# Kernel optimization log

Hardware: AMD Instinct MI355X
Metric: run time of the kernel (lower is better)

## Reference

```python
import jax, jax.numpy as jnp
import numpy as np

N_NODES = 50000
N_EDGES = 625000
D = 128          # hidden_dim
H = 8            # num_heads
DH = D // H      # head_dim
L = 4            # num_layers
F_IN = 64        # in_channels
G = 64           # num graphs
BETA = 1.0
EPS = 1e-5       # layernorm eps


def _seg_softmax(s, idx, n):
    # softmax of s over segments defined by idx (segments present in idx are never empty)
    m = jax.ops.segment_max(s, idx, num_segments=n)
    e = jnp.exp(s - m[idx])
    d = jax.ops.segment_sum(e, idx, num_segments=n)
    return e / d[idx]


def _ln(x, s, b):
    mu = jnp.mean(x, axis=-1, keepdims=True)
    var = jnp.var(x, axis=-1, keepdims=True)
    return (x - mu) / jnp.sqrt(var + EPS) * s + b


def _forward(x, edge_index, batch, node_W, node_b, cW1, cb1, cW2, cb2,
             qW, qb, kW, kb, vW, vb, oW, ob, bW, bb,
             f1W, f1b, f2W, f2b, n1s, n1b, n2s, n2b,
             outW1, outb1, outW2, outb2):
    N = x.shape[0]
    src, tgt = edge_index[0], edge_index[1]
    h = x @ node_W + node_b                              # [N, D]
    for l in range(L):
        # ---- dynamic curvature (attention-approximated Wasserstein) ----
        h_src, h_tgt = h[src], h[tgt]                    # [E, D]
        sim = jnp.sum(h_src * h_tgt, axis=-1) * BETA     # [E]
        alpha = _seg_softmax(sim, tgt, N)                # segment softmax over tgt
        dist = jnp.linalg.norm(h_src - h_tgt, axis=-1)   # [E]
        agg = jax.ops.segment_sum(alpha * dist, tgt, num_segments=N)
        curv = 1.0 - agg[tgt] / jnp.maximum(dist, 1e-6)  # [E]
        ce = jax.nn.relu(curv[:, None] @ cW1 + cb1) @ cW2 + cb2  # [E, D]
        # ---- CurvphormerLayer ----
        xn = _ln(h, n1s[l], n1b[l])
        q = (xn @ qW[l] + qb[l]).reshape(N, H, DH)
        k = (xn @ kW[l] + kb[l]).reshape(N, H, DH)
        v = (xn @ vW[l] + vb[l]).reshape(N, H, DH)
        scores = jnp.sum(q[src] * k[tgt], axis=-1) / (DH ** 0.5)  # [E, H]
        scores = scores + ce @ bW[l] + bb[l]                       # curvature bias
        probs = _seg_softmax(scores, tgt, N)                       # [E, H]
        msgs = (probs[..., None] * v[tgt]).reshape(-1, D)          # [E, D]
        aggm = jax.ops.segment_sum(msgs, src, num_segments=N)     # scatter to src
        h = h + (aggm @ oW[l] + ob[l])
        xn2 = _ln(h, n2s[l], n2b[l])
        h = h + (jax.nn.relu(xn2 @ f1W[l] + f1b[l]) @ f2W[l] + f2b[l])
    # ---- mean pool per graph ----
    counts = jnp.maximum(jax.ops.segment_sum(jnp.ones((N,), h.dtype), batch, num_segments=G), 1.0)
    g = jax.ops.segment_sum(h, batch, num_segments=G) / counts[:, None]
    return jax.nn.relu(g @ outW1 + outb1) @ outW2 + outb2


def setup_inputs() -> dict:
    keys = iter(jax.random.split(jax.random.key(0), 32))
    p = lambda shape, s=0.02: jax.random.normal(next(keys), shape, jnp.float32) * s
    x = jax.random.normal(next(keys), (N_NODES, F_IN), jnp.float32)
    edge_index = jax.random.randint(next(keys), (2, N_EDGES), 0, N_NODES)
    batch = jnp.sort(jax.random.randint(next(keys), (N_NODES,), 0, G))
    inp = {
        "x": x, "edge_index": edge_index, "batch": batch,
        "node_W": p((F_IN, D)), "node_b": p((D,)),
        "cW1": p((1, D)), "cb1": p((D,)), "cW2": p((D, D)), "cb2": p((D,)),
        "qW": p((L, D, D)), "qb": p((L, D)),
        "kW": p((L, D, D)), "kb": p((L, D)),
        "vW": p((L, D, D)), "vb": p((L, D)),
        "oW": p((L, D, D)), "ob": p((L, D)),
        "bW": p((L, D, H)), "bb": p((L, H)),
        "f1W": p((L, D, 4 * D)), "f1b": p((L, 4 * D)),
        "f2W": p((L, 4 * D, D)), "f2b": p((L, D)),
        "n1s": jnp.ones((L, D), jnp.float32), "n1b": jnp.zeros((L, D), jnp.float32),
        "n2s": jnp.ones((L, D), jnp.float32), "n2b": jnp.zeros((L, D), jnp.float32),
        "outW1": p((D, D // 2)), "outb1": p((D // 2,)),
        "outW2": p((D // 2, 1)), "outb2": p((1,)),
    }
    return inp


def reference(x, edge_index, batch, node_W, node_b, cW1, cb1, cW2, cb2,
              qW, qb, kW, kb, vW, vb, oW, ob, bW, bb,
              f1W, f1b, f2W, f2b, n1s, n1b, n2s, n2b,
              outW1, outb1, outW2, outb2):
    return _forward(x, edge_index, batch, node_W, node_b, cW1, cb1, cW2, cb2,
                    qW, qb, kW, kb, vW, vb, oW, ob, bW, bb,
                    f1W, f1b, f2W, f2b, n1s, n1b, n2s, n2b,
                    outW1, outb1, outW2, outb2)
```

## Files before the change

### kernel.cpp

```cpp
#include <hip/hip_runtime.h>

#define NN 50000
#define NE 625000
#define DD 128
#define HH 8
#define DHH 16
#define NL 4
#define FIN 64
#define NG 64
#define LN_EPS 1e-5f
#define NSEG 129
#define NT32 1563
#define NT64 782
#define NBS 196

typedef __bf16 bf16x8_t __attribute__((ext_vector_type(8)));
typedef unsigned short ushort8_t __attribute__((ext_vector_type(8)));
typedef float f32x4_t __attribute__((ext_vector_type(4)));
union BF8 { ushort8_t u; bf16x8_t b; };

__device__ __forceinline__ void fma4(float4& a, float s, float4 w) {
  a.x = fmaf(s, w.x, a.x); a.y = fmaf(s, w.y, a.y);
  a.z = fmaf(s, w.z, a.z); a.w = fmaf(s, w.w, a.w);
}
__device__ __forceinline__ unsigned short f2bf(float f) {
  unsigned u = __float_as_uint(f);
  unsigned r = ((u >> 16) & 1u) + 0x7FFFu;
  return (unsigned short)((u + r) >> 16);
}
__device__ __forceinline__ float bf2f(unsigned short u) {
  return __uint_as_float((unsigned)u << 16);
}

__device__ __forceinline__ void ln_tile_bf32(const float* __restrict__ h, int nb,
                                             const float* __restrict__ sc,
                                             const float* __restrict__ bi,
                                             ushort* xbf) {
  int tid = threadIdx.x;
  int r = tid >> 4, l16 = tid & 15;
  int nr = nb + r; if (nr >= NN) nr = NN - 1;
  const float* hp = h + (size_t)nr * DD + l16 * 8;
  float4 a0 = *(const float4*)hp;
  float4 a1 = *(const float4*)(hp + 4);
  float sum = a0.x + a0.y + a0.z + a0.w + a1.x + a1.y + a1.z + a1.w;
  float sq  = a0.x*a0.x + a0.y*a0.y + a0.z*a0.z + a0.w*a0.w
            + a1.x*a1.x + a1.y*a1.y + a1.z*a1.z + a1.w*a1.w;
#pragma unroll
  for (int off = 8; off >= 1; off >>= 1) {
    sum += __shfl_xor(sum, off, 64);
    sq  += __shfl_xor(sq,  off, 64);
  }
  float mu   = sum * (1.0f / DD);
  float var  = sq * (1.0f / DD) - mu * mu;
  float rstd = rsqrtf(var + LN_EPS);
  int d0 = l16 * 8;
  float4 s0 = *(const float4*)(sc + d0), s1 = *(const float4*)(sc + d0 + 4);
  float4 b0 = *(const float4*)(bi + d0), b1 = *(const float4*)(bi + d0 + 4);
  ushort8_t u;
  u[0] = f2bf((a0.x - mu) * rstd * s0.x + b0.x);
  u[1] = f2bf((a0.y - mu) * rstd * s0.y + b0.y);
  u[2] = f2bf((a0.z - mu) * rstd * s0.z + b0.z);
  u[3] = f2bf((a0.w - mu) * rstd * s0.w + b0.w);
  u[4] = f2bf((a1.x - mu) * rstd * s1.x + b1.x);
  u[5] = f2bf((a1.y - mu) * rstd * s1.y + b1.y);
  u[6] = f2bf((a1.z - mu) * rstd * s1.z + b1.z);
  u[7] = f2bf((a1.w - mu) * rstd * s1.w + b1.w);
  int off = (r * 256 + l16 * 16) ^ ((r & 7) << 4);
  *(ushort8_t*)((char*)xbf + off) = u;
}

__device__ __forceinline__ void ln_tile_bf64(const float* __restrict__ h, int nb,
                                             const float* __restrict__ sc,
                                             const float* __restrict__ bi,
                                             ushort* xbf) {
  int tid = threadIdx.x;
  int l16 = tid & 15;
  int d0 = l16 * 8;
  float4 s0 = *(const float4*)(sc + d0), s1 = *(const float4*)(sc + d0 + 4);
  float4 b0 = *(const float4*)(bi + d0), b1 = *(const float4*)(bi + d0 + 4);
#pragma unroll
  for (int p = 0; p < 2; p++) {
    int r = p * 32 + (tid >> 4);
    int nr = nb + r; if (nr >= NN) nr = NN - 1;
    const float* hp = h + (size_t)nr * DD + d0;
    float4 a0 = *(const float4*)hp;
    float4 a1 = *(const float4*)(hp + 4);
    float sum = a0.x + a0.y + a0.z + a0.w + a1.x + a1.y + a1.z + a1.w;
    float sq  = a0.x*a0.x + a0.y*a0.y + a0.z*a0.z + a0.w*a0.w
              + a1.x*a1.x + a1.y*a1.y + a1.z*a1.z + a1.w*a1.w;
#pragma unroll
    for (int off = 8; off >= 1; off >>= 1) {
      sum += __shfl_xor(sum, off, 64);
      sq  += __shfl_xor(sq,  off, 64);
    }
    float mu   = sum * (1.0f / DD);
    float var  = sq * (1.0f / DD) - mu * mu;
    float rstd = rsqrtf(var + LN_EPS);
    ushort8_t u;
    u[0] = f2bf((a0.x - mu) * rstd * s0.x + b0.x);
    u[1] = f2bf((a0.y - mu) * rstd * s0.y + b0.y);
    u[2] = f2bf((a0.z - mu) * rstd * s0.z + b0.z);
    u[3] = f2bf((a0.w - mu) * rstd * s0.w + b0.w);
    u[4] = f2bf((a1.x - mu) * rstd * s1.x + b1.x);
    u[5] = f2bf((a1.y - mu) * rstd * s1.y + b1.y);
    u[6] = f2bf((a1.z - mu) * rstd * s1.z + b1.z);
    u[7] = f2bf((a1.w - mu) * rstd * s1.w + b1.w);
    int off = (r * 256 + l16 * 16) ^ ((r & 7) << 4);
    *(ushort8_t*)((char*)xbf + off) = u;
  }
}

__global__ __launch_bounds__(256) void k_node_proj(const float* __restrict__ x,
                                                   const float* __restrict__ W,
                                                   const float* __restrict__ b,
                                                   float* __restrict__ h) {
  __shared__ float Wl[FIN * DD];
  __shared__ float xt[32][FIN];
  int tid = threadIdx.x;
  int nb = blockIdx.x * 32;
  for (int i = tid * 4; i < FIN * DD; i += 1024)
    *(float4*)&Wl[i] = *(const float4*)(W + i);
  for (int i = tid * 4; i < 32 * FIN; i += 1024) {
    int row = i >> 6, cc = i & 63;
    int node = nb + row; if (node >= NN) node = NN - 1;
    *(float4*)&xt[row][cc] = *(const float4*)(x + (size_t)node * FIN + cc);
  }
  __syncthreads();
  int c4 = (tid & 31) * 4;
  int r0 = (tid >> 5) * 4;
  float4 bv = *(const float4*)(b + c4);
  float4 a0 = bv, a1 = bv, a2 = bv, a3 = bv;
  for (int k = 0; k < FIN; k++) {
    float4 wv = *(const float4*)&Wl[k * DD + c4];
    fma4(a0, xt[r0][k], wv);
    fma4(a1, xt[r0 + 1][k], wv);
    fma4(a2, xt[r0 + 2][k], wv);
    fma4(a3, xt[r0 + 3][k], wv);
  }
  int n0 = nb + r0;
  if (n0 < NN)     *(float4*)(h + (size_t)n0 * DD + c4) = a0;
  if (n0 + 1 < NN) *(float4*)(h + (size_t)(n0 + 1) * DD + c4) = a1;
  if (n0 + 2 < NN) *(float4*)(h + (size_t)(n0 + 2) * DD + c4) = a2;
  if (n0 + 3 < NN) *(float4*)(h + (size_t)(n0 + 3) * DD + c4) = a3;
}

__global__ __launch_bounds__(256) void k_edge1(const int* __restrict__ src_s, const int* __restrict__ tgt_s,
                                               const float* __restrict__ h, float* __restrict__ sim,
                                               float* __restrict__ dist) {
  int gid = blockIdx.x * 256 + threadIdx.x;
  int e = gid >> 4;
  if (e >= NE) return;
  int j = gid & 15;
  int s = src_s[e], t = tgt_s[e];
  const float4* ap = (const float4*)(h + (size_t)s * DD + j * 8);
  const float4* bp = (const float4*)(h + (size_t)t * DD + j * 8);
  float4 a0 = ap[0], a1 = ap[1];
  float4 b0 = bp[0], b1 = bp[1];
  float dot = 0.f, sq = 0.f;
  dot = fmaf(a0.x, b0.x, dot); dot = fmaf(a0.y, b0.y, dot);
  dot = fmaf(a0.z, b0.z, dot); dot = fmaf(a0.w, b0.w, dot);
  dot = fmaf(a1.x, b1.x, dot); dot = fmaf(a1.y, b1.y, dot);
  dot = fmaf(a1.z, b1.z, dot); dot = fmaf(a1.w, b1.w, dot);
  float d0 = a0.x - b0.x, d1 = a0.y - b0.y, d2 = a0.z - b0.z, d3 = a0.w - b0.w;
  float d4 = a1.x - b1.x, d5 = a1.y - b1.y, d6 = a1.z - b1.z, d7 = a1.w - b1.w;
  sq = fmaf(d0, d0, sq); sq = fmaf(d1, d1, sq); sq = fmaf(d2, d2, sq); sq = fmaf(d3, d3, sq);
  sq = fmaf(d4, d4, sq); sq = fmaf(d5, d5, sq); sq = fmaf(d6, d6, sq); sq = fmaf(d7, d7, sq);
#pragma unroll
  for (int off = 8; off >= 1; off >>= 1) {
    dot += __shfl_xor(dot, off, 64);
    sq  += __shfl_xor(sq,  off, 64);
  }
  if (j == 0) {
    sim[e]  = dot;
    dist[e] = sqrtf(sq);
  }
}

__global__ __launch_bounds__(256) void k_curva(const int* __restrict__ rowstart_t,
    const int* __restrict__ eid_t, const float* __restrict__ sim,
    const float* __restrict__ dist, float* __restrict__ aggv) {
  int node = blockIdx.x * 32 + (threadIdx.x >> 3);
  if (node >= NN) return;
  int j = threadIdx.x & 7;
  int rs = rowstart_t[node], re = rowstart_t[node + 1];
  float m = -3.4e38f;
  for (int i = rs + j; i < re; i += 8) m = fmaxf(m, sim[eid_t[i]]);
#pragma unroll
  for (int off = 1; off <= 4; off <<= 1) m = fmaxf(m, __shfl_xor(m, off, 64));
  float den = 0.f, nd = 0.f;
  for (int i = rs + j; i < re; i += 8) {
    int e = eid_t[i];
    float ev = expf(sim[e] - m);
    den += ev;
    nd = fmaf(ev, dist[e], nd);
  }
#pragma unroll
  for (int off = 1; off <= 4; off <<= 1) {
    den += __shfl_xor(den, off, 64);
    nd  += __shfl_xor(nd,  off, 64);
  }
  if (j == 0) aggv[node] = den > 0.f ? nd / den : 0.f;
}

__global__ __launch_bounds__(512) void k_ln_qkv(const float* __restrict__ h,
    const float* __restrict__ n1s_l, const float* __restrict__ n1b_l,
    const ushort* __restrict__ qkvT_l,
    const float* __restrict__ qb_l, const float* __restrict__ kb_l, const float* __restrict__ vb_l,
    ushort* __restrict__ q, ushort* __restrict__ kk, ushort* __restrict__ v) {
  __shared__ __align__(16) ushort xbf[32 * DD];
  int nb = blockIdx.x * 32;
  ln_tile_bf32(h, nb, n1s_l, n1b_l, xbf);
  __syncthreads();
  int lane = threadIdx.x & 63;
  int w = threadIdx.x >> 6;
  int g = lane >> 4, c = lane & 15;
  int xr = (c & 7) << 4;
  char* xb = (char*)xbf;
  BF8 a[2][4];
#pragma unroll
  for (int nt = 0; nt < 2; nt++)
#pragma unroll
    for (int kt = 0; kt < 4; kt++)
      a[nt][kt].u = *(ushort8_t*)(xb + (((nt * 16 + c) * 256 + kt * 64 + g * 16) ^ xr));
#pragma unroll
  for (int ti = 0; ti < 3; ti++) {
    int t = w * 3 + ti;
    int m = t >> 3;
    int colb = (t & 7) * 16;
    const float* bias = (m == 0 ? qb_l : (m == 1 ? kb_l : vb_l));
    float4 bv = *(const float4*)(bias + colb + g * 4);
    f32x4_t acc0 = {bv.x, bv.y, bv.z, bv.w};
    f32x4_t acc1 = acc0;
    const ushort* wp = qkvT_l + (size_t)(m * DD + colb + c) * DD + g * 8;
#pragma unroll
    for (int kt = 0; kt < 4; kt++) {
      BF8 b; b.u = *(const ushort8_t*)(wp + kt * 32);
      acc0 = __builtin_amdgcn_mfma_f32_16x16x32_bf16(b.b, a[0][kt].b, acc0, 0, 0, 0);
      acc1 = __builtin_amdgcn_mfma_f32_16x16x32_bf16(b.b, a[1][kt].b, acc1, 0, 0, 0);
    }
    ushort* out = (m == 0 ? q : (m == 1 ? kk : v));
    int n0 = nb + c;
    if (n0 < NN) {
      ushort4 o; o.x = f2bf(acc0[0]); o.y = f2bf(acc0[1]); o.z = f2bf(acc0[2]); o.w = f2bf(acc0[3]);
      *(ushort4*)(out + (size_t)n0 * DD + colb + g * 4) = o;
    }
    int n1 = nb + 16 + c;
    if (n1 < NN) {
      ushort4 o; o.x = f2bf(acc1[0]); o.y = f2bf(acc1[1]); o.z = f2bf(acc1[2]); o.w = f2bf(acc1[3]);
      *(ushort4*)(out + (size_t)n1 * DD + colb + g * 4) = o;
    }
  }
}

__global__ __launch_bounds__(256) void k_scores(const int* __restrict__ src_s, const int* __restrict__ tgt_s,
    const ushort* __restrict__ q, const ushort* __restrict__ k,
    const float* __restrict__ dist, const float* __restrict__ aggv,
    const float* __restrict__ bp_g,
    const float* __restrict__ slope_l, const float* __restrict__ inter_l,
    float* __restrict__ escore) {
  __shared__ float lsl[NSEG * HH], lin[NSEG * HH], bp[DD];
  __shared__ float lcurv[32];
  __shared__ int   lseg[32];
  int tid = threadIdx.x;
  for (int idx = tid; idx < NSEG * HH; idx += 256) { lsl[idx] = slope_l[idx]; lin[idx] = inter_l[idx]; }
  if (tid < DD) bp[tid] = bp_g[tid];
  __syncthreads();
  int eb = blockIdx.x * 32;
  if (tid < 32) {
    int e = eb + tid;
    if (e < NE) {
      int t = tgt_s[e];
      float curv = 1.0f - aggv[t] / fmaxf(dist[e], 1e-6f);
      int lo = 0, hi = DD;
      while (lo < hi) { int mid = (lo + hi) >> 1; if (bp[mid] < curv) lo = mid + 1; else hi = mid; }
      lcurv[tid] = curv;
      lseg[tid] = lo;
    }
  }
  __syncthreads();
  int gi = blockIdx.x * 256 + tid;
  if (gi >= NE * HH) return;
  int i = gi >> 3, hh = gi & 7;
  int s = src_s[i], t = tgt_s[i];
  int li = tid >> 3;
  float curv = lcurv[li];
  int seg = lseg[li];
  float bias = fmaf(lsl[seg * HH + hh], curv, lin[seg * HH + hh]);
  const ushort8_t* qp = (const ushort8_t*)(q + (size_t)s * DD + hh * DHH);
  const ushort8_t* kp = (const ushort8_t*)(k + (size_t)t * DD + hh * DHH);
  float dot = 0.f;
#pragma unroll
  for (int ii = 0; ii < 2; ii++) {
    ushort8_t a = qp[ii], b = kp[ii];
#pragma unroll
    for (int jj = 0; jj < 8; jj++) dot = fmaf(bf2f(a[jj]), bf2f(b[jj]), dot);
  }
  escore[gi] = dot * 0.25f + bias;
  (void)t;
}

__global__ __launch_bounds__(256) void k_softmax_t(const int* __restrict__ rowstart_t,
    const int* __restrict__ eid_t, const float* __restrict__ escore, float2* __restrict__ msd) {
  int node = blockIdx.x * 32 + (threadIdx.x >> 3);
  if (node >= NN) return;
  int hh = threadIdx.x & 7;
  int rs = rowstart_t[node], re = rowstart_t[node + 1];
  float m = -3.4e38f;
  int i = rs;
  for (; i + 4 <= re; i += 4) {
    int e0 = eid_t[i], e1 = eid_t[i + 1], e2 = eid_t[i + 2], e3 = eid_t[i + 3];
    float s0 = escore[e0 * HH + hh];
    float s1 = escore[e1 * HH + hh];
    float s2 = escore[e2 * HH + hh];
    float s3 = escore[e3 * HH + hh];
    m = fmaxf(m, s0); m = fmaxf(m, s1); m = fmaxf(m, s2); m = fmaxf(m, s3);
  }
  for (; i < re; i++) m = fmaxf(m, escore[eid_t[i] * HH + hh]);
  float sum = 0.f;
  i = rs;
  for (; i + 4 <= re; i += 4) {
    int e0 = eid_t[i], e1 = eid_t[i + 1], e2 = eid_t[i + 2], e3 = eid_t[i + 3];
    float p0 = expf(escore[e0 * HH + hh] - m);
    float p1 = expf(escore[e1 * HH + hh] - m);
    float p2 = expf(escore[e2 * HH + hh] - m);
    float p3 = expf(escore[e3 * HH + hh] - m);
    sum += p0; sum += p1; sum += p2; sum += p3;
  }
  for (; i < re; i++) sum += expf(escore[eid_t[i] * HH + hh] - m);
  float2 o; o.x = m; o.y = sum > 0.f ? 1.0f / sum : 0.f;
  msd[(size_t)node * HH + hh] = o;
}

__global__ __launch_bounds__(256) void k_agg(const int* __restrict__ tgt_s,
    const int* __restrict__ rowstart,
    const float* __restrict__ escore, const float2* __restrict__ msd,
    const ushort* __restrict__ v, ushort* __restrict__ aggmb) {
  int wave = (blockIdx.x * 256 + threadIdx.x) >> 6;
  int lane = threadIdx.x & 63;
  int rs = rowstart[wave], re = rowstart[wave + 1];
  int hh = lane >> 3;
  int d = lane * 2;
  float a0 = 0.f, a1 = 0.f;
  int i = rs;
  for (; i + 4 <= re; i += 4) {
    int t0 = tgt_s[i], t1 = tgt_s[i + 1], t2 = tgt_s[i + 2], t3 = tgt_s[i + 3];
    float e0 = escore[(i    ) * HH + hh];
    float e1 = escore[(i + 1) * HH + hh];
    float e2 = escore[(i + 2) * HH + hh];
    float e3 = escore[(i + 3) * HH + hh];
    float2 m0 = msd[(size_t)t0 * HH + hh], m1 = msd[(size_t)t1 * HH + hh];
    float2 m2 = msd[(size_t)t2 * HH + hh], m3 = msd[(size_t)t3 * HH + hh];
    ushort2 v0 = *(const ushort2*)(v + (size_t)t0 * DD + d);
    ushort2 v1 = *(const ushort2*)(v + (size_t)t1 * DD + d);
    ushort2 v2 = *(const ushort2*)(v + (size_t)t2 * DD + d);
    ushort2 v3 = *(const ushort2*)(v + (size_t)t3 * DD + d);
    float p0 = expf(e0 - m0.x) * m0.y;
    float p1 = expf(e1 - m1.x) * m1.y;
    float p2 = expf(e2 - m2.x) * m2.y;
    float p3 = expf(e3 - m3.x) * m3.y;
    a0 = fmaf(p0, bf2f(v0.x), a0); a1 = fmaf(p0, bf2f(v0.y), a1);
    a0 = fmaf(p1, bf2f(v1.x), a0); a1 = fmaf(p1, bf2f(v1.y), a1);
    a0 = fmaf(p2, bf2f(v2.x), a0); a1 = fmaf(p2, bf2f(v2.y), a1);
    a0 = fmaf(p3, bf2f(v3.x), a0); a1 = fmaf(p3, bf2f(v3.y), a1);
  }
  for (; i < re; i++) {
    int t = tgt_s[i];
    float2 md = msd[(size_t)t * HH + hh];
    float prob = expf(escore[i * HH + hh] - md.x) * md.y;
    ushort2 vv = *(const ushort2*)(v + (size_t)t * DD + d);
    a0 = fmaf(prob, bf2f(vv.x), a0);
    a1 = fmaf(prob, bf2f(vv.y), a1);
  }
  ushort2 o; o.x = f2bf(a0); o.y = f2bf(a1);
  *(ushort2*)(aggmb + (size_t)wave * DD + d) = o;
}

__global__ __launch_bounds__(512) void k_update_o(const ushort* __restrict__ aggmb,
    const ushort* __restrict__ oT_l, const float* __restrict__ ob_l, float* __restrict__ h) {
  int nb = blockIdx.x * 32;
  int lane = threadIdx.x & 63, w = threadIdx.x >> 6;
  int g = lane >> 4, c = lane & 15;
  BF8 a[2][4];
#pragma unroll
  for (int nt = 0; nt < 2; nt++) {
    int na = nb + nt * 16 + c; if (na >= NN) na = NN - 1;
    const ushort* ap = aggmb + (size_t)na * DD + g * 8;
#pragma unroll
    for (int kt = 0; kt < 4; kt++) a[nt][kt].u = *(const ushort8_t*)(ap + kt * 32);
  }
  int colb = w * 16;
  float4 bv = *(const float4*)(ob_l + colb + g * 4);
  f32x4_t acc0 = {bv.x, bv.y, bv.z, bv.w};
  f32x4_t acc1 = acc0;
  const ushort* wp = oT_l + (size_t)(colb + c) * DD + g * 8;
#pragma unroll
  for (int kt = 0; kt < 4; kt++) {
    BF8 b; b.u = *(const ushort8_t*)(wp + kt * 32);
    acc0 = __builtin_amdgcn_mfma_f32_16x16x32_bf16(b.b, a[0][kt].b, acc0, 0, 0, 0);
    acc1 = __builtin_amdgcn_mfma_f32_16x16x32_bf16(b.b, a[1][kt].b, acc1, 0, 0, 0);
  }
#pragma unroll
  for (int nt = 0; nt < 2; nt++) {
    int node = nb + nt * 16 + c;
    if (node < NN) {
      float* hp = h + (size_t)node * DD + colb + g * 4;
      float4 hv = *(const float4*)hp;
      f32x4_t& acc = nt ? acc1 : acc0;
      hv.x += acc[0]; hv.y += acc[1]; hv.z += acc[2]; hv.w += acc[3];
      *(float4*)hp = hv;
    }
  }
}

__global__ __launch_bounds__(512) void k_ffn(const float* __restrict__ n2s_l, const float* __restrict__ n2b_l,
    const ushort* __restrict__ f1T_l, const float* __restrict__ f1b_l,
    const ushort* __restrict__ f2T_l, const float* __restrict__ f2b_l,
    float* __restrict__ h) {
  __shared__ __align__(16) ushort xbf[64 * DD];
  __shared__ __align__(16) ushort tbf[64 * 256];
  int nb = blockIdx.x * 64;
  ln_tile_bf64(h, nb, n2s_l, n2b_l, xbf);
  __syncthreads();
  int lane = threadIdx.x & 63, w = threadIdx.x >> 6;
  int g = lane >> 4, c = lane & 15;
  int xr = (c & 7) << 4;
  char* xb = (char*)xbf;
  char* tb = (char*)tbf;
  BF8 a[4][4];
#pragma unroll
  for (int nt = 0; nt < 4; nt++)
#pragma unroll
    for (int kt = 0; kt < 4; kt++)
      a[nt][kt].u = *(ushort8_t*)(xb + (((nt * 16 + c) * 256 + kt * 64 + g * 16) ^ xr));
  int colb2 = w * 16;
  float4 bv2 = *(const float4*)(f2b_l + colb2 + g * 4);
  f32x4_t o0 = {bv2.x, bv2.y, bv2.z, bv2.w};
  f32x4_t o1 = o0, o2 = o0, o3 = o0;
#pragma unroll
  for (int ch = 0; ch < 2; ch++) {
    if (ch) __syncthreads();
#pragma unroll
    for (int ti = 0; ti < 2; ti++) {
      int ctile = w * 2 + ti;
      int col = ch * 256 + ctile * 16;
      float4 bv = *(const float4*)(f1b_l + col + g * 4);
      f32x4_t ac0 = {bv.x, bv.y, bv.z, bv.w};
      f32x4_t ac1 = ac0, ac2 = ac0, ac3 = ac0;
      const ushort* wp = f1T_l + (size_t)(col + c) * DD + g * 8;
#pragma unroll
      for (int kt = 0; kt < 4; kt++) {
        BF8 b; b.u = *(const ushort8_t*)(wp + kt * 32);
        ac0 = __builtin_amdgcn_mfma_f32_16x16x32_bf16(b.b, a[0][kt].b, ac0, 0, 0, 0);
        ac1 = __builtin_amdgcn_mfma_f32_16x16x32_bf16(b.b, a[1][kt].b, ac1, 0, 0, 0);
        ac2 = __builtin_amdgcn_mfma_f32_16x16x32_bf16(b.b, a[2][kt].b, ac2, 0, 0, 0);
        ac3 = __builtin_amdgcn_mfma_f32_16x16x32_bf16(b.b, a[3][kt].b, ac3, 0, 0, 0);
      }
      int colL = (ctile * 16 + g * 4) * 2;
      {
        int row = c;
        ushort4 o4; o4.x = f2bf(fmaxf(ac0[0], 0.f)); o4.y = f2bf(fmaxf(ac0[1], 0.f));
        o4.z = f2bf(fmaxf(ac0[2], 0.f)); o4.w = f2bf(fmaxf(ac0[3], 0.f));
        *(ushort4*)(tb + ((row * 512 + colL) ^ ((row & 7) << 4))) = o4;
      }
      {
        int row = 16 + c;
        ushort4 o4; o4.x = f2bf(fmaxf(ac1[0], 0.f)); o4.y = f2bf(fmaxf(ac1[1], 0.f));
        o4.z = f2bf(fmaxf(ac1[2], 0.f)); o4.w = f2bf(fmaxf(ac1[3], 0.f));
        *(ushort4*)(tb + ((row * 512 + colL) ^ ((row & 7) << 4))) = o4;
      }
      {
        int row = 32 + c;
        ushort4 o4; o4.x = f2bf(fmaxf(ac2[0], 0.f)); o4.y = f2bf(fmaxf(ac2[1], 0.f));
        o4.z = f2bf(fmaxf(ac2[2], 0.f)); o4.w = f2bf(fmaxf(ac2[3], 0.f));
        *(ushort4*)(tb + ((row * 512 + colL) ^ ((row & 7) << 4))) = o4;
      }
      {
        int row = 48 + c;
        ushort4 o4; o4.x = f2bf(fmaxf(ac3[0], 0.f)); o4.y = f2bf(fmaxf(ac3[1], 0.f));
        o4.z = f2bf(fmaxf(ac3[2], 0.f)); o4.w = f2bf(fmaxf(ac3[3], 0.f));
        *(ushort4*)(tb + ((row * 512 + colL) ^ ((row & 7) << 4))) = o4;
      }
    }
    __syncthreads();
    const ushort* wp2 = f2T_l + (size_t)(colb2 + c) * 512 + ch * 256 + g * 8;
#pragma unroll
    for (int kt = 0; kt < 8; kt++) {
      BF8 b; b.u = *(const ushort8_t*)(wp2 + kt * 32);
      BF8 t0; t0.u = *(ushort8_t*)(tb + (((c) * 512 + kt * 64 + g * 16) ^ xr));
      BF8 t1; t1.u = *(ushort8_t*)(tb + (((16 + c) * 512 + kt * 64 + g * 16) ^ xr));
      BF8 t2; t2.u = *(ushort8_t*)(tb + (((32 + c) * 512 + kt * 64 + g * 16) ^ xr));
      BF8 t3; t3.u = *(ushort8_t*)(tb + (((48 + c) * 512 + kt * 64 + g * 16) ^ xr));
      o0 = __builtin_amdgcn_mfma_f32_16x16x32_bf16(b.b, t0.b, o0, 0, 0, 0);
      o1 = __builtin_amdgcn_mfma_f32_16x16x32_bf16(b.b, t1.b, o1, 0, 0, 0);
      o2 = __builtin_amdgcn_mfma_f32_16x16x32_bf16(b.b, t2.b, o2, 0, 0, 0);
      o3 = __builtin_amdgcn_mfma_f32_16x16x32_bf16(b.b, t3.b, o3, 0, 0, 0);
    }
  }
  {
    int node = nb + c;
    if (node < NN) {
      float* hp = h + (size_t)node * DD + colb2 + g * 4;
      float4 hv = *(const float4*)hp;
      hv.x += o0[0]; hv.y += o0[1]; hv.z += o0[2]; hv.w += o0[3];
      *(float4*)hp = hv;
    }
  }
  {
    int node = nb + 16 + c;
    if (node < NN) {
      float* hp = h + (size_t)node * DD + colb2 + g * 4;
      float4 hv = *(const float4*)hp;
      hv.x += o1[0]; hv.y += o1[1]; hv.z += o1[2]; hv.w += o1[3];
      *(float4*)hp = hv;
    }
  }
  {
    int node = nb + 32 + c;
    if (node < NN) {
      float* hp = h + (size_t)node * DD + colb2 + g * 4;
      float4 hv = *(const float4*)hp;
      hv.x += o2[0]; hv.y += o2[1]; hv.z += o2[2]; hv.w += o2[3];
      *(float4*)hp = hv;
    }
  }
  {
    int node = nb + 48 + c;
    if (node < NN) {
      float* hp = h + (size_t)node * DD + colb2 + g * 4;
      float4 hv = *(const float4*)hp;
      hv.x += o3[0]; hv.y += o3[1]; hv.z += o3[2]; hv.w += o3[3];
      *(float4*)hp = hv;
    }
  }
}

template <int K, int C>
__global__ void k_wt(const float* __restrict__ W, ushort* __restrict__ WT, int nm, int dstride) {
  int idx = blockIdx.x * 256 + threadIdx.x;
  if (idx >= K * C * nm) return;
  int mi = idx / (K * C), rem = idx - mi * (K * C);
  int cc = rem / K, kk2 = rem - cc * K;
  WT[(size_t)mi * dstride + cc * K + kk2] = f2bf(W[(size_t)mi * K * C + (size_t)kk2 * C + cc]);
}

__global__ void k_hist(const int* __restrict__ idxs, int* __restrict__ cnt) {
  int e = blockIdx.x * 256 + threadIdx.x;
  if (e < NE) atomicAdd(cnt + idxs[e], 1);
}

__global__ __launch_bounds__(256) void k_scan_blk(const int* __restrict__ cnt, int* __restrict__ bsum) {
  __shared__ int red[256];
  int tid = threadIdx.x;
  int idx = blockIdx.x * 256 + tid;
  red[tid] = (idx < NN) ? cnt[idx] : 0;
  __syncthreads();
  for (int off = 128; off >= 1; off >>= 1) {
    if (tid < off) red[tid] += red[tid + off];
    __syncthreads();
  }
  if (tid == 0) bsum[blockIdx.x] = red[0];
}

__global__ __launch_bounds__(256) void k_scan_top(const int* __restrict__ bsum,
                                                  int* __restrict__ boff, int* __restrict__ rowstart) {
  __shared__ int ps[256];
  int t = threadIdx.x;
  int v = (t < NBS) ? bsum[t] : 0;
  ps[t] = v;
  __syncthreads();
  for (int off = 1; off < 256; off <<= 1) {
    int x = (t >= off) ? ps[t - off] : 0;
    __syncthreads();
    ps[t] += x;
    __syncthreads();
  }
  boff[t] = ps[t] - v;
  if (t == 255) rowstart[NN] = ps[255];
}

__global__ __launch_bounds__(256) void k_scan_fin(const int* __restrict__ cnt,
                                                  const int* __restrict__ boff, int* __restrict__ rowstart) {
  __shared__ int ps[256];
  int t = threadIdx.x;
  int idx = blockIdx.x * 256 + t;
  int v = (idx < NN) ? cnt[idx] : 0;
  ps[t] = v;
  __syncthreads();
  for (int off = 1; off < 256; off <<= 1) {
    int x = (t >= off) ? ps[t - off] : 0;
    __syncthreads();
    ps[t] += x;
    __syncthreads();
  }
  if (idx < NN) rowstart[idx] = boff[blockIdx.x] + ps[t] - v;
}

__global__ void k_fill(const int* __restrict__ src, const int* __restrict__ tgt,
                       const int* __restrict__ rowstart,
                       int* __restrict__ cur, int* __restrict__ src_s, int* __restrict__ tgt_s) {
  int e = blockIdx.x * 256 + threadIdx.x;
  if (e >= NE) return;
  int s = src[e];
  int p = atomicAdd(cur + s, 1);
  int pos = rowstart[s] + p;
  src_s[pos] = s;
  tgt_s[pos] = tgt[e];
}

__global__ void k_fill_t(const int* __restrict__ tgt_s, const int* __restrict__ rowstart_t,
                         int* __restrict__ cur_t, int* __restrict__ eid_t) {
  int i = blockIdx.x * 256 + threadIdx.x;
  if (i >= NE) return;
  int t = tgt_s[i];
  int p = atomicAdd(cur_t + t, 1);
  eid_t[rowstart_t[t] + p] = i;
}

__global__ __launch_bounds__(64) void k_mbias_par(const float* __restrict__ cW2, const float* __restrict__ cb2,
                                                  const float* __restrict__ bW, const float* __restrict__ bb,
                                                  float* __restrict__ M, float* __restrict__ base) {
  int bid = blockIdx.x;
  int l = bid >> 7, d = bid & 127;
  int lane = threadIdx.x;
  int hh = lane >> 3, j0 = lane & 7;
  const float* bWl = bW + (size_t)l * DD * HH;
  float acc = 0.f;
#pragma unroll
  for (int t = 0; t < 16; t++) {
    int k = j0 + t * 8;
    acc = fmaf(cW2[d * DD + k], bWl[k * HH + hh], acc);
  }
#pragma unroll
  for (int off = 1; off <= 4; off <<= 1) acc += __shfl_xor(acc, off, 64);
  if (j0 == 0) M[(size_t)l * DD * HH + d * HH + hh] = acc;
  if (d == 0) {
    float bacc = 0.f;
#pragma unroll
    for (int t = 0; t < 16; t++) {
      int k = j0 + t * 8;
      bacc = fmaf(cb2[k], bWl[k * HH + hh], bacc);
    }
#pragma unroll
    for (int off = 1; off <= 4; off <<= 1) bacc += __shfl_xor(bacc, off, 64);
    if (j0 == 0) base[l * HH + hh] = bacc + bb[l * HH + hh];
  }
}

__global__ __launch_bounds__(128) void k_bp(const float* __restrict__ cW1, const float* __restrict__ cb1,
                                            float* __restrict__ bpg, int* __restrict__ posg) {
  __shared__ float x[DD], bp[DD];
  int tid = threadIdx.x;
  float c1v = cW1[tid], cbv = cb1[tid];
  x[tid] = (c1v == 0.f) ? __builtin_inff() : (-cbv / c1v);
  __syncthreads();
  float xv = x[tid]; int p = 0;
  for (int j = 0; j < DD; j++) {
    float xj = x[j];
    if (xj < xv || (xj == xv && j < tid)) p++;
  }
  bp[p] = xv;
  posg[tid] = p;
  __syncthreads();
  bpg[tid] = bp[tid];
}

__global__ __launch_bounds__(64) void k_pwl_tab(const float* __restrict__ cW1, const float* __restrict__ cb1,
    const int* __restrict__ posg, const float* __restrict__ Mb, const float* __restrict__ basel,
    float* __restrict__ slopeg, float* __restrict__ interg) {
  int bid = blockIdx.x;
  int l = bid / NSEG, s = bid - l * NSEG;
  int lane = threadIdx.x;
  int hh = lane >> 3, j0 = lane & 7;
  const float* M = Mb + (size_t)l * DD * HH;
  float sl = 0.f, in = 0.f;
#pragma unroll
  for (int t = 0; t < 16; t++) {
    int d = j0 + t * 8;
    float cv = cW1[d], cbv = cb1[d];
    int p = posg[d];
    bool act = (cv == 0.f) ? (cbv > 0.f) : ((cv > 0.f) ? (p < s) : (p >= s));
    float m = act ? M[d * HH + hh] : 0.f;
    sl = fmaf(cv, m, sl);
    in = fmaf(cbv, m, in);
  }
#pragma unroll
  for (int off = 1; off <= 4; off <<= 1) {
    sl += __shfl_xor(sl, off, 64);
    in += __shfl_xor(in, off, 64);
  }
  if (j0 == 0) {
    size_t o = (size_t)l * NSEG * HH + s * HH + hh;
    slopeg[o] = sl;
    interg[o] = in + basel[l * HH + hh];
  }
}

__global__ void k_bounds(const int* __restrict__ batch, int* __restrict__ gstart, int* __restrict__ gend) {
  int n = blockIdx.x * 256 + threadIdx.x;
  if (n >= NN) return;
  int b = batch[n];
  if (n == 0 || batch[n - 1] != b) gstart[b] = n;
  if (n == NN - 1 || batch[n + 1] != b) gend[b] = n + 1;
}

__global__ __launch_bounds__(256) void k_pool_part(const float* __restrict__ h,
    const int* __restrict__ batch, float* __restrict__ gpool) {
  int tid = threadIdx.x;
  int d = tid & 127, sub = tid >> 7;
  int n0 = blockIdx.x * 256;
  int nend = n0 + 256; if (nend > NN) nend = NN;
  float run = 0.f; int gcur = -1;
  for (int n = n0 + sub; n < nend; n += 2) {
    int g = batch[n];
    if (g != gcur) {
      if (gcur >= 0) atomicAdd(gpool + (size_t)gcur * DD + d, run);
      run = 0.f; gcur = g;
    }
    run += h[(size_t)n * DD + d];
  }
  if (gcur >= 0) atomicAdd(gpool + (size_t)gcur * DD + d, run);
}

__global__ __launch_bounds__(256) void k_head(const float* __restrict__ gpool,
    const int* __restrict__ gstart, const int* __restrict__ gend,
    const float* __restrict__ W1, const float* __restrict__ b1,
    const float* __restrict__ W2, const float* __restrict__ b2, float* __restrict__ out) {
  __shared__ float mid[NG * 64];
  int tid = threadIdx.x;
  for (int idx = tid; idx < NG * 64; idx += 256) {
    int g = idx >> 6, j = idx & 63;
    int cnt = gend[g] - gstart[g]; if (cnt < 1) cnt = 1;
    float rc = 1.0f / (float)cnt;
    float acc = 0.f;
    for (int d = 0; d < DD; d++) acc = fmaf(gpool[g * DD + d], W1[d * 64 + j], acc);
    mid[idx] = fmaxf(fmaf(acc, rc, b1[j]), 0.f);
  }
  __syncthreads();
  if (tid < NG) {
    float acc = b2[0];
    for (int j = 0; j < 64; j++) acc = fmaf(mid[tid * 64 + j], W2[j], acc);
    out[tid] = acc;
  }
}

extern "C" void kernel_launch(void* const* d_in, const int* in_sizes, int n_in,
                              void* d_out, int out_size, void* d_ws, size_t ws_size,
                              hipStream_t stream) {
  const float* x      = (const float*)d_in[0];
  const int*   ei     = (const int*)d_in[1];
  const int*   batch  = (const int*)d_in[2];
  const float* node_W = (const float*)d_in[3];
  const float* node_b = (const float*)d_in[4];
  const float* cW1    = (const float*)d_in[5];
  const float* cb1    = (const float*)d_in[6];
  const float* cW2    = (const float*)d_in[7];
  const float* cb2    = (const float*)d_in[8];
  const float* qW     = (const float*)d_in[9];
  const float* qb     = (const float*)d_in[10];
  const float* kW     = (const float*)d_in[11];
  const float* kb     = (const float*)d_in[12];
  const float* vW     = (const float*)d_in[13];
  const float* vb     = (const float*)d_in[14];
  const float* oW     = (const float*)d_in[15];
  const float* ob     = (const float*)d_in[16];
  const float* bW     = (const float*)d_in[17];
  const float* bb     = (const float*)d_in[18];
  const float* f1W    = (const float*)d_in[19];
  const float* f1b    = (const float*)d_in[20];
  const float* f2W    = (const float*)d_in[21];
  const float* f2b    = (const float*)d_in[22];
  const float* n1s    = (const float*)d_in[23];
  const float* n1b    = (const float*)d_in[24];
  const float* n2s    = (const float*)d_in[25];
  const float* n2b    = (const float*)d_in[26];
  const float* outW1  = (const float*)d_in[27];
  const float* outb1  = (const float*)d_in[28];
  const float* outW2  = (const float*)d_in[29];
  const float* outb2  = (const float*)d_in[30];

  const int* src = ei;
  const int* tgt = ei + NE;

  char* wp = (char*)d_ws;
  auto alloc = [&](size_t bytes) { void* p = (void*)wp; wp += (bytes + 255) & ~(size_t)255; return p; };
  float*    h       = (float*)alloc((size_t)NN * DD * 4);
  ushort*   q       = (ushort*)alloc((size_t)NN * DD * 2);
  ushort*   kk      = (ushort*)alloc((size_t)NN * DD * 2);
  ushort*   v       = (ushort*)alloc((size_t)NN * DD * 2);
  ushort*   aggmb   = (ushort*)alloc((size_t)NN * DD * 2);
  float*    sim     = (float*)alloc((size_t)NE * 4);
  float*    dist    = (float*)alloc((size_t)NE * 4);
  float*    escore  = (float*)alloc((size_t)NE * HH * 4);
  float2*   msd     = (float2*)alloc((size_t)NN * HH * 8);
  float*    aggv    = (float*)alloc((size_t)NN * 4);
  float*    Mb      = (float*)alloc((size_t)NL * DD * HH * 4);
  float*    basel   = (float*)alloc((size_t)NL * HH * 4);
  float*    bpg     = (float*)alloc((size_t)DD * 4);
  int*      posg    = (int*)alloc((size_t)DD * 4);
  float*    slopeg  = (float*)alloc((size_t)NL * NSEG * HH * 4);
  float*    interg  = (float*)alloc((size_t)NL * NSEG * HH * 4);
  int*      rowstart= (int*)alloc((size_t)(NN + 1) * 4);
  int*      rowstart_t = (int*)alloc((size_t)(NN + 1) * 4);
  int*      eid_t   = (int*)alloc((size_t)NE * 4);
  int*      src_s   = (int*)alloc((size_t)NE * 4);
  int*      tgt_s   = (int*)alloc((size_t)NE * 4);
  int*      cnt     = (int*)alloc((size_t)NN * 4);
  int*      cur     = (int*)alloc((size_t)NN * 4);
  int*      cnt_t   = (int*)alloc((size_t)NN * 4);
  int*      cur_t   = (int*)alloc((size_t)NN * 4);
  int*      bsum    = (int*)alloc((size_t)NBS * 4);
  int*      boff    = (int*)alloc((size_t)256 * 4);
  int*      gstart  = (int*)alloc((size_t)NG * 4);
  int*      gend    = (int*)alloc((size_t)NG * 4);
  float*    gpool   = (float*)alloc((size_t)NG * DD * 4);
  ushort*   qkvT    = (ushort*)alloc((size_t)NL * 3 * DD * DD * 2);
  ushort*   oT      = (ushort*)alloc((size_t)NL * DD * DD * 2);
  ushort*   f1T     = (ushort*)alloc((size_t)NL * DD * 512 * 2);
  ushort*   f2T     = (ushort*)alloc((size_t)NL * 512 * DD * 2);
  (void)in_sizes; (void)n_in; (void)out_size; (void)ws_size;

  hipMemsetAsync(cnt, 0, NN * 4, stream);
  hipMemsetAsync(cur, 0, NN * 4, stream);
  hipMemsetAsync(cnt_t, 0, NN * 4, stream);
  hipMemsetAsync(cur_t, 0, NN * 4, stream);
  hipMemsetAsync(gstart, 0, NG * 4, stream);
  hipMemsetAsync(gend, 0, NG * 4, stream);
  hipMemsetAsync(gpool, 0, NG * DD * 4, stream);
  k_hist<<<(NE + 255) / 256, 256, 0, stream>>>(src, cnt);
  k_scan_blk<<<NBS, 256, 0, stream>>>(cnt, bsum);
  k_scan_top<<<1, 256, 0, stream>>>(bsum, boff, rowstart);
  k_scan_fin<<<NBS, 256, 0, stream>>>(cnt, boff, rowstart);
  k_fill<<<(NE + 255) / 256, 256, 0, stream>>>(src, tgt, rowstart, cur, src_s, tgt_s);
  k_hist<<<(NE + 255) / 256, 256, 0, stream>>>(tgt, cnt_t);
  k_scan_blk<<<NBS, 256, 0, stream>>>(cnt_t, bsum);
  k_scan_top<<<1, 256, 0, stream>>>(bsum, boff, rowstart_t);
  k_scan_fin<<<NBS, 256, 0, stream>>>(cnt_t, boff, rowstart_t);
  k_fill_t<<<(NE + 255) / 256, 256, 0, stream>>>(tgt_s, rowstart_t, cur_t, eid_t);
  k_mbias_par<<<NL * DD, 64, 0, stream>>>(cW2, cb2, bW, bb, Mb, basel);
  k_bp<<<1, 128, 0, stream>>>(cW1, cb1, bpg, posg);
  k_pwl_tab<<<NL * NSEG, 64, 0, stream>>>(cW1, cb1, posg, Mb, basel, slopeg, interg);
  k_bounds<<<(NN + 255) / 256, 256, 0, stream>>>(batch, gstart, gend);
  k_wt<DD, DD><<<(NL * DD * DD + 255) / 256, 256, 0, stream>>>(qW, qkvT,               NL, 3 * DD * DD);
  k_wt<DD, DD><<<(NL * DD * DD + 255) / 256, 256, 0, stream>>>(kW, qkvT + DD * DD,     NL, 3 * DD * DD);
  k_wt<DD, DD><<<(NL * DD * DD + 255) / 256, 256, 0, stream>>>(vW, qkvT + 2 * DD * DD, NL, 3 * DD * DD);
  k_wt<DD, DD><<<(NL * DD * DD + 255) / 256, 256, 0, stream>>>(oW, oT, NL, DD * DD);
  k_wt<DD, 512><<<(NL * DD * 512 + 255) / 256, 256, 0, stream>>>(f1W, f1T, NL, DD * 512);
  k_wt<512, DD><<<(NL * DD * 512 + 255) / 256, 256, 0, stream>>>(f2W, f2T, NL, DD * 512);
  k_node_proj<<<NT32, 256, 0, stream>>>(x, node_W, node_b, h);

  for (int l = 0; l < NL; l++) {
    k_edge1<<<(NE * 16 + 255) / 256, 256, 0, stream>>>(src_s, tgt_s, h, sim, dist);
    k_curva<<<NT32, 256, 0, stream>>>(rowstart_t, eid_t, sim, dist, aggv);
    k_ln_qkv<<<NT32, 512, 0, stream>>>(h, n1s + l * DD, n1b + l * DD,
        qkvT + (size_t)l * 3 * DD * DD,
        qb + l * DD, kb + l * DD, vb + l * DD, q, kk, v);
    k_scores<<<(NE * HH + 255) / 256, 256, 0, stream>>>(src_s, tgt_s, q, kk,
        dist, aggv, bpg,
        slopeg + (size_t)l * NSEG * HH, interg + (size_t)l * NSEG * HH,
        escore);
    k_softmax_t<<<NT32, 256, 0, stream>>>(rowstart_t, eid_t, escore, msd);
    k_agg<<<NN / 4, 256, 0, stream>>>(tgt_s, rowstart, escore, msd, v, aggmb);
    k_update_o<<<NT32, 512, 0, stream>>>(aggmb, oT + (size_t)l * DD * DD, ob + l * DD, h);
    k_ffn<<<NT64, 512, 0, stream>>>(n2s + l * DD, n2b + l * DD,
        f1T + (size_t)l * DD * 512, f1b + (size_t)l * 4 * DD,
        f2T + (size_t)l * 512 * DD, f2b + l * DD, h);
  }
  k_pool_part<<<(NN + 255) / 256, 256, 0, stream>>>(h, batch, gpool);
  k_head<<<1, 256, 0, stream>>>(gpool, gstart, gend, outW1, outb1, outW2, outb2, (float*)d_out);
}
```

Baseline: 1.407 ms.

## Fuse attention output projection into FFN kernel with residual held in LDS

Merges the output-projection/residual-update kernel into the FFN kernel. The post-attention residual is kept in a shared-memory tile, then layer-normed and fed to the FFN, and the final residual is written once. This removes one kernel launch per layer and one round trip of the hidden state through global memory. In exchange the kernel uses more LDS (an extra fp32 tile, with the bf16 buffers aliased), which may lower occupancy, and it adds extra barriers.

Result: faster. 1.372 ms (-2.5%).

```diff
diff --git a/kernel.cpp b/kernel.cpp
--- a/kernel.cpp
+++ b/kernel.cpp
@@ -13,6 +13,7 @@
 #define NT32 1563
 #define NT64 782
 #define NBS 196
+#define HLP 132
 
 typedef __bf16 bf16x8_t __attribute__((ext_vector_type(8)));
 typedef unsigned short ushort8_t __attribute__((ext_vector_type(8)));
@@ -67,47 +68,6 @@
   u[7] = f2bf((a1.w - mu) * rstd * s1.w + b1.w);
   int off = (r * 256 + l16 * 16) ^ ((r & 7) << 4);
   *(ushort8_t*)((char*)xbf + off) = u;
-}
-
-__device__ __forceinline__ void ln_tile_bf64(const float* __restrict__ h, int nb,
-                                             const float* __restrict__ sc,
-                                             const float* __restrict__ bi,
-                                             ushort* xbf) {
-  int tid = threadIdx.x;
-  int l16 = tid & 15;
-  int d0 = l16 * 8;
-  float4 s0 = *(const float4*)(sc + d0), s1 = *(const float4*)(sc + d0 + 4);
-  float4 b0 = *(const float4*)(bi + d0), b1 = *(const float4*)(bi + d0 + 4);
-#pragma unroll
-  for (int p = 0; p < 2; p++) {
-    int r = p * 32 + (tid >> 4);
-    int nr = nb + r; if (nr >= NN) nr = NN - 1;
-    const float* hp = h + (size_t)nr * DD + d0;
-    float4 a0 = *(const float4*)hp;
-    float4 a1 = *(const float4*)(hp + 4);
-    float sum = a0.x + a0.y + a0.z + a0.w + a1.x + a1.y + a1.z + a1.w;
-    float sq  = a0.x*a0.x + a0.y*a0.y + a0.z*a0.z + a0.w*a0.w
-              + a1.x*a1.x + a1.y*a1.y + a1.z*a1.z + a1.w*a1.w;
-#pragma unroll
-    for (int off = 8; off >= 1; off >>= 1) {
-      sum += __shfl_xor(sum, off, 64);
-      sq  += __shfl_xor(sq,  off, 64);
-    }
-    float mu   = sum * (1.0f / DD);
-    float var  = sq * (1.0f / DD) - mu * mu;
-    float rstd = rsqrtf(var + LN_EPS);
-    ushort8_t u;
-    u[0] = f2bf((a0.x - mu) * rstd * s0.x + b0.x);
-    u[1] = f2bf((a0.y - mu) * rstd * s0.y + b0.y);
-    u[2] = f2bf((a0.z - mu) * rstd * s0.z + b0.z);
-    u[3] = f2bf((a0.w - mu) * rstd * s0.w + b0.w);
-    u[4] = f2bf((a1.x - mu) * rstd * s1.x + b1.x);
-    u[5] = f2bf((a1.y - mu) * rstd * s1.y + b1.y);
-    u[6] = f2bf((a1.z - mu) * rstd * s1.z + b1.z);
-    u[7] = f2bf((a1.w - mu) * rstd * s1.w + b1.w);
-    int off = (r * 256 + l16 * 16) ^ ((r & 7) << 4);
-    *(ushort8_t*)((char*)xbf + off) = u;
-  }
 }
 
 __global__ __launch_bounds__(256) void k_node_proj(const float* __restrict__ x,
@@ -375,65 +335,96 @@
   *(ushort2*)(aggmb + (size_t)wave * DD + d) = o;
 }
 
-__global__ __launch_bounds__(512) void k_update_o(const ushort* __restrict__ aggmb,
-    const ushort* __restrict__ oT_l, const float* __restrict__ ob_l, float* __restrict__ h) {
-  int nb = blockIdx.x * 32;
-  int lane = threadIdx.x & 63, w = threadIdx.x >> 6;
-  int g = lane >> 4, c = lane & 15;
-  BF8 a[2][4];
-#pragma unroll
-  for (int nt = 0; nt < 2; nt++) {
-    int na = nb + nt * 16 + c; if (na >= NN) na = NN - 1;
-    const ushort* ap = aggmb + (size_t)na * DD + g * 8;
-#pragma unroll
-    for (int kt = 0; kt < 4; kt++) a[nt][kt].u = *(const ushort8_t*)(ap + kt * 32);
-  }
-  int colb = w * 16;
-  float4 bv = *(const float4*)(ob_l + colb + g * 4);
-  f32x4_t acc0 = {bv.x, bv.y, bv.z, bv.w};
-  f32x4_t acc1 = acc0;
-  const ushort* wp = oT_l + (size_t)(colb + c) * DD + g * 8;
-#pragma unroll
-  for (int kt = 0; kt < 4; kt++) {
-    BF8 b; b.u = *(const ushort8_t*)(wp + kt * 32);
-    acc0 = __builtin_amdgcn_mfma_f32_16x16x32_bf16(b.b, a[0][kt].b, acc0, 0, 0, 0);
-    acc1 = __builtin_amdgcn_mfma_f32_16x16x32_bf16(b.b, a[1][kt].b, acc1, 0, 0, 0);
-  }
-#pragma unroll
-  for (int nt = 0; nt < 2; nt++) {
-    int node = nb + nt * 16 + c;
-    if (node < NN) {
-      float* hp = h + (size_t)node * DD + colb + g * 4;
-      float4 hv = *(const float4*)hp;
-      f32x4_t& acc = nt ? acc1 : acc0;
-      hv.x += acc[0]; hv.y += acc[1]; hv.z += acc[2]; hv.w += acc[3];
-      *(float4*)hp = hv;
-    }
-  }
-}
-
-__global__ __launch_bounds__(512) void k_ffn(const float* __restrict__ n2s_l, const float* __restrict__ n2b_l,
+__global__ __launch_bounds__(512) void k_attn_ffn(const ushort* __restrict__ aggmb,
+    const ushort* __restrict__ oT_l, const float* __restrict__ ob_l,
+    const float* __restrict__ n2s_l, const float* __restrict__ n2b_l,
     const ushort* __restrict__ f1T_l, const float* __restrict__ f1b_l,
     const ushort* __restrict__ f2T_l, const float* __restrict__ f2b_l,
     float* __restrict__ h) {
-  __shared__ __align__(16) ushort xbf[64 * DD];
-  __shared__ __align__(16) ushort tbf[64 * 256];
+  __shared__ float hL[64 * HLP];
+  __shared__ __align__(16) char ubuf[64 * 256 * 2];
+  ushort* xbf = (ushort*)ubuf;
+  char* xb = ubuf;
+  char* tb = ubuf;
   int nb = blockIdx.x * 64;
-  ln_tile_bf64(h, nb, n2s_l, n2b_l, xbf);
-  __syncthreads();
-  int lane = threadIdx.x & 63, w = threadIdx.x >> 6;
+  int tid = threadIdx.x;
+  int lane = tid & 63, w = tid >> 6;
   int g = lane >> 4, c = lane & 15;
+  int colb = w * 16;
   int xr = (c & 7) << 4;
-  char* xb = (char*)xbf;
-  char* tb = (char*)tbf;
+  {
+    float4 obv = *(const float4*)(ob_l + colb + g * 4);
+    const ushort* wp = oT_l + (size_t)(colb + c) * DD + g * 8;
+    BF8 b0, b1, b2, b3;
+    b0.u = *(const ushort8_t*)(wp);
+    b1.u = *(const ushort8_t*)(wp + 32);
+    b2.u = *(const ushort8_t*)(wp + 64);
+    b3.u = *(const ushort8_t*)(wp + 96);
+#pragma unroll
+    for (int nt = 0; nt < 4; nt++) {
+      int node = nb + nt * 16 + c;
+      int na = node < NN ? node : NN - 1;
+      const ushort* ap = aggmb + (size_t)na * DD + g * 8;
+      BF8 a0, a1, a2, a3;
+      a0.u = *(const ushort8_t*)(ap);
+      a1.u = *(const ushort8_t*)(ap + 32);
+      a2.u = *(const ushort8_t*)(ap + 64);
+      a3.u = *(const ushort8_t*)(ap + 96);
+      f32x4_t acc = {obv.x, obv.y, obv.z, obv.w};
+      acc = __builtin_amdgcn_mfma_f32_16x16x32_bf16(b0.b, a0.b, acc, 0, 0, 0);
+      acc = __builtin_amdgcn_mfma_f32_16x16x32_bf16(b1.b, a1.b, acc, 0, 0, 0);
+      acc = __builtin_amdgcn_mfma_f32_16x16x32_bf16(b2.b, a2.b, acc, 0, 0, 0);
+      acc = __builtin_amdgcn_mfma_f32_16x16x32_bf16(b3.b, a3.b, acc, 0, 0, 0);
+      float4 hv = *(const float4*)(h + (size_t)na * DD + colb + g * 4);
+      hv.x += acc[0]; hv.y += acc[1]; hv.z += acc[2]; hv.w += acc[3];
+      *(float4*)&hL[(nt * 16 + c) * HLP + colb + g * 4] = hv;
+    }
+  }
+  __syncthreads();
+  {
+    int l16 = tid & 15;
+    int d0 = l16 * 8;
+    float4 s0 = *(const float4*)(n2s_l + d0), s1 = *(const float4*)(n2s_l + d0 + 4);
+    float4 bb0 = *(const float4*)(n2b_l + d0), bb1 = *(const float4*)(n2b_l + d0 + 4);
+#pragma unroll
+    for (int p = 0; p < 2; p++) {
+      int r = p * 32 + (tid >> 4);
+      const float* hp = &hL[r * HLP + d0];
+      float4 a0 = *(const float4*)hp;
+      float4 a1 = *(const float4*)(hp + 4);
+      float sum = a0.x + a0.y + a0.z + a0.w + a1.x + a1.y + a1.z + a1.w;
+      float sq  = a0.x*a0.x + a0.y*a0.y + a0.z*a0.z + a0.w*a0.w
+                + a1.x*a1.x + a1.y*a1.y + a1.z*a1.z + a1.w*a1.w;
+#pragma unroll
+      for (int off = 8; off >= 1; off >>= 1) {
+        sum += __shfl_xor(sum, off, 64);
+        sq  += __shfl_xor(sq,  off, 64);
+      }
+      float mu   = sum * (1.0f / DD);
+      float var  = sq * (1.0f / DD) - mu * mu;
+      float rstd = rsqrtf(var + LN_EPS);
+      ushort8_t u;
+      u[0] = f2bf((a0.x - mu) * rstd * s0.x + bb0.x);
+      u[1] = f2bf((a0.y - mu) * rstd * s0.y + bb0.y);
+      u[2] = f2bf((a0.z - mu) * rstd * s0.z + bb0.z);
+      u[3] = f2bf((a0.w - mu) * rstd * s0.w + bb0.w);
+      u[4] = f2bf((a1.x - mu) * rstd * s1.x + bb1.x);
+      u[5] = f2bf((a1.y - mu) * rstd * s1.y + bb1.y);
+      u[6] = f2bf((a1.z - mu) * rstd * s1.z + bb1.z);
+      u[7] = f2bf((a1.w - mu) * rstd * s1.w + bb1.w);
+      int off = (r * 256 + l16 * 16) ^ ((r & 7) << 4);
+      *(ushort8_t*)(xb + off) = u;
+    }
+  }
+  __syncthreads();
   BF8 a[4][4];
 #pragma unroll
   for (int nt = 0; nt < 4; nt++)
 #pragma unroll
     for (int kt = 0; kt < 4; kt++)
       a[nt][kt].u = *(ushort8_t*)(xb + (((nt * 16 + c) * 256 + kt * 64 + g * 16) ^ xr));
-  int colb2 = w * 16;
-  float4 bv2 = *(const float4*)(f2b_l + colb2 + g * 4);
+  __syncthreads();
+  float4 bv2 = *(const float4*)(f2b_l + colb + g * 4);
   f32x4_t o0 = {bv2.x, bv2.y, bv2.z, bv2.w};
   f32x4_t o1 = o0, o2 = o0, o3 = o0;
 #pragma unroll
@@ -482,7 +473,7 @@
       }
     }
     __syncthreads();
-    const ushort* wp2 = f2T_l + (size_t)(colb2 + c) * 512 + ch * 256 + g * 8;
+    const ushort* wp2 = f2T_l + (size_t)(colb + c) * 512 + ch * 256 + g * 8;
 #pragma unroll
     for (int kt = 0; kt < 8; kt++) {
       BF8 b; b.u = *(const ushort8_t*)(wp2 + kt * 32);
@@ -499,37 +490,37 @@
   {
     int node = nb + c;
     if (node < NN) {
-      float* hp = h + (size_t)node * DD + colb2 + g * 4;
-      float4 hv = *(const float4*)hp;
+      const float* lp = &hL[c * HLP + colb + g * 4];
+      float4 hv = *(const float4*)lp;
       hv.x += o0[0]; hv.y += o0[1]; hv.z += o0[2]; hv.w += o0[3];
-      *(float4*)hp = hv;
+      *(float4*)(h + (size_t)node * DD + colb + g * 4) = hv;
     }
   }
   {
     int node = nb + 16 + c;
     if (node < NN) {
-      float* hp = h + (size_t)node * DD + colb2 + g * 4;
-      float4 hv = *(const float4*)hp;
+      const float* lp = &hL[(16 + c) * HLP + colb + g * 4];
+      float4 hv = *(const float4*)lp;
       hv.x += o1[0]; hv.y += o1[1]; hv.z += o1[2]; hv.w += o1[3];
-      *(float4*)hp = hv;
+      *(float4*)(h + (size_t)node * DD + colb + g * 4) = hv;
     }
   }
   {
     int node = nb + 32 + c;
     if (node < NN) {
-      float* hp = h + (size_t)node * DD + colb2 + g * 4;
-      float4 hv = *(const float4*)hp;
+      const float* lp = &hL[(32 + c) * HLP + colb + g * 4];
+      float4 hv = *(const float4*)lp;
       hv.x += o2[0]; hv.y += o2[1]; hv.z += o2[2]; hv.w += o2[3];
-      *(float4*)hp = hv;
+      *(float4*)(h + (size_t)node * DD + colb + g * 4) = hv;
     }
   }
   {
     int node = nb + 48 + c;
     if (node < NN) {
-      float* hp = h + (size_t)node * DD + colb2 + g * 4;
-      float4 hv = *(const float4*)hp;
+      const float* lp = &hL[(48 + c) * HLP + colb + g * 4];
+      float4 hv = *(const float4*)lp;
       hv.x += o3[0]; hv.y += o3[1]; hv.z += o3[2]; hv.w += o3[3];
-      *(float4*)hp = hv;
+      *(float4*)(h + (size_t)node * DD + colb + g * 4) = hv;
     }
   }
 }
@@ -860,8 +851,8 @@
         escore);
     k_softmax_t<<<NT32, 256, 0, stream>>>(rowstart_t, eid_t, escore, msd);
     k_agg<<<NN / 4, 256, 0, stream>>>(tgt_s, rowstart, escore, msd, v, aggmb);
-    k_update_o<<<NT32, 512, 0, stream>>>(aggmb, oT + (size_t)l * DD * DD, ob + l * DD, h);
-    k_ffn<<<NT64, 512, 0, stream>>>(n2s + l * DD, n2b + l * DD,
+    k_attn_ffn<<<NT64, 512, 0, stream>>>(aggmb, oT + (size_t)l * DD * DD, ob + l * DD,
+        n2s + l * DD, n2b + l * DD,
         f1T + (size_t)l * DD * 512, f1b + (size_t)l * 4 * DD,
         f2T + (size_t)l * 512 * DD, f2b + l * DD, h);
   }
```
